# Optimization experiments

Hardware: AMD Instinct MI355X
Metric: run time of the kernel (lower is better)

Reference implementation:

```python
import jax, jax.numpy as jnp
import numpy as np

RES, RES_, STRIDE = 28, 14, 2
H, KD, AR = 8, 16, 4
SCALE = KD ** -0.5
EPS = 1e-5


def make_bias_idxs(res=RES, res_=RES_, stride=STRIDE):
    pts = [(i, j) for i in range(res) for j in range(res)]
    pts_ = [(i, j) for i in range(res_) for j in range(res_)]
    offs, idxs = {}, []
    for p1 in pts_:
        for p2 in pts:
            off = (abs(p1[0] * stride - p2[0]), abs(p1[1] * stride - p2[1]))
            if off not in offs:
                offs[off] = len(offs)
            idxs.append(offs[off])
    return np.array(idxs, dtype=np.int32).reshape(len(pts_), len(pts)), len(offs)


def setup_inputs() -> dict:
    key = jax.random.key(0)
    ks = jax.random.split(key, 16)
    idxs, n_off = make_bias_idxs()  # n_off == 784
    B, N, C = 128, RES * RES, 256
    d_kv, d_q, d_p, d_pin = 640, 128, 384, 512
    return {
        "hidden_state": jax.random.normal(ks[0], (B, N, C), jnp.float32),
        "w_kv": jax.random.normal(ks[1], (d_kv, C), jnp.float32) * 0.05,
        "kv_gamma": jax.random.uniform(ks[2], (d_kv,), jnp.float32, 0.5, 1.5),
        "kv_beta": jax.random.normal(ks[3], (d_kv,), jnp.float32) * 0.1,
        "kv_mean": jax.random.normal(ks[4], (d_kv,), jnp.float32) * 0.1,
        "kv_var": jax.random.uniform(ks[5], (d_kv,), jnp.float32, 0.5, 1.5),
        "w_q": jax.random.normal(ks[6], (d_q, C), jnp.float32) * 0.05,
        "q_gamma": jax.random.uniform(ks[7], (d_q,), jnp.float32, 0.5, 1.5),
        "q_beta": jax.random.normal(ks[8], (d_q,), jnp.float32) * 0.1,
        "q_mean": jax.random.normal(ks[9], (d_q,), jnp.float32) * 0.1,
        "q_var": jax.random.uniform(ks[10], (d_q,), jnp.float32, 0.5, 1.5),
        "w_proj": jax.random.normal(ks[11], (d_p, d_pin), jnp.float32) * 0.05,
        "p_gamma": jax.random.uniform(ks[12], (d_p,), jnp.float32, 0.5, 1.5),
        "p_beta": jax.random.normal(ks[13], (d_p,), jnp.float32) * 0.1,
        "p_mean": jax.random.normal(ks[14], (d_p,), jnp.float32) * 0.1,
        "p_var": jax.random.uniform(ks[15], (d_p,), jnp.float32, 0.5, 1.5),
        "attention_biases": jax.random.normal(jax.random.fold_in(key, 99), (H, n_off), jnp.float32),
        "attention_bias_idxs": jnp.asarray(idxs),
    }


def _bn(x, gamma, beta, mean, var):
    # eval-mode BatchNorm1d over last dim
    return (x - mean) * (gamma * jax.lax.rsqrt(var + EPS)) + beta


def _hardswish(x):
    return x * jnp.clip(x + 3.0, 0.0, 6.0) * (1.0 / 6.0)


def reference(hidden_state, w_kv, kv_gamma, kv_beta, kv_mean, kv_var,
              w_q, q_gamma, q_beta, q_mean, q_var,
              w_proj, p_gamma, p_beta, p_mean, p_var,
              attention_biases, attention_bias_idxs):
    B, N, C = hidden_state.shape
    N_ = RES_ * RES_
    # kv: [B, N, 640] -> key [B,H,N,KD], value [B,H,N,AR*KD]
    kv = _bn(hidden_state @ w_kv.T, kv_gamma, kv_beta, kv_mean, kv_var)
    kv = kv.reshape(B, N, H, KD + AR * KD)
    k = jnp.transpose(kv[..., :KD], (0, 2, 1, 3))          # [B,H,N,KD]
    v = jnp.transpose(kv[..., KD:], (0, 2, 1, 3))          # [B,H,N,AR*KD]
    # strided query subsample on the spatial grid
    hs = hidden_state.reshape(B, RES, RES, C)[:, ::STRIDE, ::STRIDE].reshape(B, N_, C)
    q = _bn(hs @ w_q.T, q_gamma, q_beta, q_mean, q_var)
    q = jnp.transpose(q.reshape(B, N_, H, KD), (0, 2, 1, 3))  # [B,H,N_,KD]
    bias = attention_biases[:, attention_bias_idxs]           # [H,N_,N] gathered
    attn = jnp.einsum('bhqd,bhkd->bhqk', q, k) * SCALE + bias
    attn = jax.nn.softmax(attn, axis=-1)
    out = jnp.einsum('bhqk,bhkd->bhqd', attn, v)              # [B,H,N_,AR*KD]
    out = jnp.transpose(out, (0, 2, 1, 3)).reshape(B, N_, H * AR * KD)
    out = _bn(_hardswish(out) @ w_proj.T, p_gamma, p_beta, p_mean, p_var)
    return out
```

## Files before the change

kernel.cpp:

```cpp
#include <hip/hip_runtime.h>

typedef _Float16 f16;
typedef __attribute__((ext_vector_type(2))) _Float16 f16x2;
typedef __attribute__((ext_vector_type(4))) _Float16 f16x4;
typedef __attribute__((ext_vector_type(8))) _Float16 f16x8;
typedef __attribute__((ext_vector_type(4))) float fvec4;
typedef __attribute__((ext_vector_type(4))) float f32x4;
typedef __attribute__((ext_vector_type(16))) float f32x16;
typedef __attribute__((ext_vector_type(4))) unsigned int uint4v;

#define NKEY 784
#define NKEYP 800
#define NQ 196
#define NQP 224
#define LOG2E 1.442695041f
#define SC2   0.360673760f
#define THR2  11.5415603f

static __device__ __forceinline__ f32x4 mfma16(f16x8 a, f16x8 b, f32x4 c) {
    return __builtin_amdgcn_mfma_f32_16x16x32_f16(a, b, c, 0, 0, 0);
}
static __device__ __forceinline__ f32x16 mfma32(f16x8 a, f16x8 b, f32x16 c) {
    return __builtin_amdgcn_mfma_f32_32x32x16_f16(a, b, c, 0, 0, 0);
}
static __device__ __forceinline__ unsigned pkrtz(float a, float b) {
    return __builtin_bit_cast(unsigned, __builtin_amdgcn_cvt_pkrtz(a, b));
}
static __device__ __forceinline__ f32x16 z16() {
    f32x16 v;
#pragma unroll
    for (int i = 0; i < 16; ++i) v[i] = 0.f;
    return v;
}

__global__ void prep_scales_all(const float* __restrict__ kg, const float* __restrict__ kb,
                                const float* __restrict__ km, const float* __restrict__ kvv,
                                const float* __restrict__ qg, const float* __restrict__ qb,
                                const float* __restrict__ qm, const float* __restrict__ qv,
                                const float* __restrict__ pg, const float* __restrict__ pb,
                                const float* __restrict__ pm, const float* __restrict__ pv,
                                float* __restrict__ sb) {
    int i = blockIdx.x * 256 + threadIdx.x;
    if (i < 640) {
        float s = kg[i] * rsqrtf(kvv[i] + 1e-5f);
        sb[i] = s; sb[640 + i] = kb[i] - km[i] * s;
    } else if (i < 768) {
        int j = i - 640;
        float s = qg[j] * rsqrtf(qv[j] + 1e-5f);
        sb[1280 + j] = s * SC2;
        sb[1408 + j] = (qb[j] - qm[j] * s) * SC2;
    } else if (i < 1152) {
        int j = i - 768;
        float s = pg[j] * rsqrtf(pv[j] + 1e-5f);
        sb[1536 + j] = s; sb[1920 + j] = pb[j] - pm[j] * s;
    }
}

__global__ void conv_w(const float* __restrict__ wkv, const float* __restrict__ wq,
                       const float* __restrict__ wp, f16* __restrict__ out) {
    int i = blockIdx.x * 256 + threadIdx.x;
    const float* src;
    f16* dst;
    int kc, n, K;
    if (i < 20480)      { int j = i;         kc = j / 640, n = j - kc * 640; src = wkv; dst = out + (size_t)j * 8;            K = 256; }
    else if (i < 24576) { int j = i - 20480; kc = j / 128, n = j - kc * 128; src = wq;  dst = out + 163840 + (size_t)j * 8;   K = 256; }
    else                { int j = i - 24576; kc = j / 384, n = j - kc * 384; src = wp;  dst = out + 196608 + (size_t)j * 8;   K = 512; }
    const float* s = src + (size_t)n * K + kc * 8;
    fvec4 v0 = *(const fvec4*)s;
    fvec4 v1 = *(const fvec4*)(s + 4);
    f16x8 h;
    h[0] = (f16)v0[0]; h[1] = (f16)v0[1]; h[2] = (f16)v0[2]; h[3] = (f16)v0[3];
    h[4] = (f16)v1[0]; h[5] = (f16)v1[1]; h[6] = (f16)v1[2]; h[7] = (f16)v1[3];
    *(f16x8*)dst = h;
}

__global__ void prep_bias(const float* __restrict__ biases, const int* __restrict__ idxs,
                          f16* __restrict__ biasS, int n_off) {
    int tid = blockIdx.x * 256 + threadIdx.x;
    const int r = tid & 15;
    const int lane = (tid >> 4) & 63;
    const int g = tid >> 10;
    const int kbk = g % 25;
    const int tmp = g / 25;
    const int qt = tmp % 7;
    const int h = tmp / 7;
    const int q = qt * 32 + (lane & 31);
    const int key = kbk * 32 + (r & 3) + 8 * (r >> 2) + 4 * (lane >> 5);
    float v;
    if (key >= NKEY)  v = -30000.f;
    else if (q < NQ)  v = biases[h * n_off + idxs[q * NKEY + key]] * LOG2E;
    else              v = 0.f;
    biasS[tid] = (f16)v;
}

template <int MODE>
__global__ __launch_bounds__(256) void gemm_db(
        const void* __restrict__ Ap, const f16x8* __restrict__ Wg,
        const float* __restrict__ sc, const float* __restrict__ sh,
        void* __restrict__ OutA, f16* __restrict__ OutV) {
    constexpr int K     = (MODE == 2) ? 512 : 256;
    constexpr int KS    = K / 32;
    constexpr int CHUNK = (MODE == 2) ? 16 : 32;
    constexpr int NFR   = CHUNK / 16;
    constexpr int NT    = (MODE == 0) ? 640 : (MODE == 1 ? 128 : 384);
    constexpr int NCH   = (MODE == 0) ? 20 : (MODE == 1 ? 4 : 12);
    constexpr int UNITS = (K / 8) * CHUNK;
    constexpr int SR    = UNITS / 256;

    __shared__ f16x8 Wl[2][UNITS];

    const int t = threadIdx.x;
    const int lane = t & 63, wid = t >> 6;
    const int fr = lane & 15, kg = lane >> 4;
    const int m0 = blockIdx.x * 64;
    const int nb0 = blockIdx.y * (NCH * CHUNK);
    const int mrow = m0 + wid * 16 + fr;

    size_t arow;
    if constexpr (MODE == 1) {
        int b = mrow / 196, nn = mrow - b * 196;
        arow = (size_t)b * 784 + (nn / 14) * 56 + (nn % 14) * 2;
    } else {
        arow = (size_t)mrow;
    }
    f16x8 af[KS];
#pragma unroll
    for (int ks = 0; ks < KS; ++ks) {
        if constexpr (MODE == 2) {
            af[ks] = *(const f16x8*)((const f16*)Ap + arow * K + ks * 32 + kg * 8);
        } else {
            const float* a = (const float*)Ap + arow * 256 + ks * 32 + kg * 8;
            fvec4 v0 = *(const fvec4*)a;
            fvec4 v1 = *(const fvec4*)(a + 4);
            f16x8 hv;
            hv[0] = (f16)v0[0]; hv[1] = (f16)v0[1]; hv[2] = (f16)v0[2]; hv[3] = (f16)v0[3];
            hv[4] = (f16)v1[0]; hv[5] = (f16)v1[1]; hv[6] = (f16)v1[2]; hv[7] = (f16)v1[3];
            af[ks] = hv;
        }
    }

#pragma unroll
    for (int rr = 0; rr < SR; ++rr) {
        const int idx = rr * 256 + t;
        Wl[0][idx] = Wg[(size_t)(idx / CHUNK) * NT + nb0 + (idx % CHUNK)];
    }
    __syncthreads();

    const int rg = kg * 4;
    int cur = 0;
    for (int c = 0; c < NCH; ++c) {
        const int n0c = nb0 + c * CHUNK;

        f16x8 nx0, nx1, nx2, nx3;
        if (c + 1 < NCH) {
            const int n0n = n0c + CHUNK;
            nx0 = Wg[(size_t)((0 * 256 + t) / CHUNK) * NT + n0n + ((0 * 256 + t) % CHUNK)];
            if constexpr (SR > 1)
                nx1 = Wg[(size_t)((1 * 256 + t) / CHUNK) * NT + n0n + ((1 * 256 + t) % CHUNK)];
            if constexpr (SR > 2) {
                nx2 = Wg[(size_t)((2 * 256 + t) / CHUNK) * NT + n0n + ((2 * 256 + t) % CHUNK)];
                nx3 = Wg[(size_t)((3 * 256 + t) / CHUNK) * NT + n0n + ((3 * 256 + t) % CHUNK)];
            }
        }

        f32x4 acc[NFR];
#pragma unroll
        for (int j = 0; j < NFR; ++j) acc[j] = (f32x4){0.f, 0.f, 0.f, 0.f};
#pragma unroll
        for (int ks = 0; ks < KS; ++ks) {
            f16x8 bfr[NFR];
#pragma unroll
            for (int nf = 0; nf < NFR; ++nf)
                bfr[nf] = Wl[cur][(ks * 4 + kg) * CHUNK + nf * 16 + fr];
#pragma unroll
            for (int nf = 0; nf < NFR; ++nf)
                acc[nf] = mfma16(af[ks], bfr[nf], acc[nf]);
        }

        const int mbase = m0 + wid * 16 + rg;
#pragma unroll
        for (int nf = 0; nf < NFR; ++nf) {
            const int n = n0c + nf * 16 + fr;
            const float scn = sc[n], shn = sh[n];
            if constexpr (MODE == 0) {
                const int b = mbase / 784;
                const int nn = mbase - b * 784;
                const int hd = n / 80;
                const int cc = n - hd * 80;
                const size_t bh = (size_t)(b * 8 + hd);
                if (cc < 16) {
#pragma unroll
                    for (int r = 0; r < 4; ++r) {
                        float y = acc[nf][r] * scn + shn;
                        ((f16*)OutA)[(bh * NKEYP + nn + r) * 16 + cc] = (f16)y;
                    }
                } else {
                    const int kbk = nn >> 5, sH = (nn >> 4) & 1;
                    const int kq = (nn >> 2) & 3;
                    const int slot = ((((kq & 1) << 1) | (kq >> 1)) << 2) | (nn & 3);
                    f16x4 pv;
#pragma unroll
                    for (int r = 0; r < 4; ++r) pv[r] = (f16)(acc[nf][r] * scn + shn);
                    *(f16x4*)(OutV + ((bh * 25 + kbk) * 2 + sH) * 1024 + (cc - 16) * 16 + slot) = pv;
                }
            } else if constexpr (MODE == 1) {
                const int b = mbase / 196;
                const int nn = mbase - b * 196;
                const int hd = n >> 4, cc = n & 15;
                const size_t bh = (size_t)(b * 8 + hd);
#pragma unroll
                for (int r = 0; r < 4; ++r) {
                    float y = acc[nf][r] * scn + shn;
                    ((f16*)OutA)[(bh * NQP + nn + r) * 16 + cc] = (f16)y;
                }
            } else {
#pragma unroll
                for (int r = 0; r < 4; ++r) {
                    float y = acc[nf][r] * scn + shn;
                    ((float*)OutA)[(size_t)(mbase + r) * 384 + n] = y;
                }
            }
        }

        if (c + 1 < NCH) {
            Wl[cur ^ 1][0 * 256 + t] = nx0;
            if constexpr (SR > 1)
                Wl[cur ^ 1][1 * 256 + t] = nx1;
            if constexpr (SR > 2) {
                Wl[cur ^ 1][2 * 256 + t] = nx2;
                Wl[cur ^ 1][3 * 256 + t] = nx3;
            }
            __syncthreads();
            cur ^= 1;
        }
    }
}

__global__ __launch_bounds__(448) void attn_fused(const f16* __restrict__ kb,
                                                  const f16* __restrict__ vtb,
                                                  const f16* __restrict__ qw,
                                                  const f16* __restrict__ biasS,
                                                  f16* __restrict__ ao) {
    const int bh = blockIdx.x;
    const int b = bh >> 3, h = bh & 7;
    const int wid = threadIdx.x >> 6;
    const int lane = threadIdx.x & 63;
    const int l31 = lane & 31;
    const int hh = lane >> 5;
    const int q0 = wid * 32;

    const f16x8 bq = *(const f16x8*)(qw + ((size_t)bh * NQP + q0 + l31) * 16 + hh * 8);
    const f16* kpp = kb + (size_t)bh * (NKEYP * 16) + (size_t)l31 * 16 + hh * 8;
    const f16* cbp = biasS + ((size_t)(h * 7 + wid) * 25 * 64 + lane) * 16;
    const f16* vkb = vtb + (size_t)bh * 51200 + l31 * 16 + hh * 8;

    float mrun = -1e30f;
    float lsum = 0.f;
    f32x16 o0 = z16(), o1 = z16();

    f32x16 sn;
    {
        const f16x8* bp = (const f16x8*)cbp;
        f16x8 b0 = bp[0], b1 = bp[1];
        f32x16 ci;
#pragma unroll
        for (int r = 0; r < 8; ++r) { ci[r] = (float)b0[r]; ci[8 + r] = (float)b1[r]; }
        sn = mfma32(*(const f16x8*)kpp, bq, ci);
    }

#pragma unroll 1
    for (int kbi = 0; kbi < 25; ++kbi) {
        f32x16 s = sn;
        if (kbi + 1 < 25) {
            kpp += 512; cbp += 1024;
            const f16x8* bp = (const f16x8*)cbp;
            f16x8 b0 = bp[0], b1 = bp[1];
            f32x16 ci;
#pragma unroll
            for (int r = 0; r < 8; ++r) { ci[r] = (float)b0[r]; ci[8 + r] = (float)b1[r]; }
            sn = mfma32(*(const f16x8*)kpp, bq, ci);
        }
        f16x8 bv00 = *(const f16x8*)(vkb);
        f16x8 bv01 = *(const f16x8*)(vkb + 512);
        f16x8 bv10 = *(const f16x8*)(vkb + 1024);
        f16x8 bv11 = *(const f16x8*)(vkb + 1536);
        vkb += 2048;

        float m0v = fmaxf(fmaxf(s[0], s[1]), fmaxf(s[2], s[3]));
        float m1v = fmaxf(fmaxf(s[4], s[5]), fmaxf(s[6], s[7]));
        float m2v = fmaxf(fmaxf(s[8], s[9]), fmaxf(s[10], s[11]));
        float m3v = fmaxf(fmaxf(s[12], s[13]), fmaxf(s[14], s[15]));
        float cmax = fmaxf(fmaxf(m0v, m1v), fmaxf(m2v, m3v));
        cmax = fmaxf(cmax, __shfl_xor(cmax, 32));
        if (__any(cmax > mrun + THR2)) {
            float mnew = fmaxf(mrun, cmax);
            float f = exp2f(mrun - mnew);
            mrun = mnew;
            lsum *= f;
#pragma unroll
            for (int r = 0; r < 16; ++r) {
                const int cr = (r & 3) + ((r >> 2) << 3) + (hh << 2);
                float fr2 = __shfl(f, cr);
                o0[r] *= fr2;
                o1[r] *= fr2;
            }
        }
        float pr[16];
        float psum = 0.f;
#pragma unroll
        for (int r = 0; r < 16; ++r) {
            pr[r] = exp2f(s[r] - mrun);
            psum += pr[r];
        }
        lsum += psum;
        uint4v w0, w1;
        w0[0] = pkrtz(pr[0], pr[1]);   w0[1] = pkrtz(pr[2], pr[3]);
        w0[2] = pkrtz(pr[4], pr[5]);   w0[3] = pkrtz(pr[6], pr[7]);
        w1[0] = pkrtz(pr[8], pr[9]);   w1[1] = pkrtz(pr[10], pr[11]);
        w1[2] = pkrtz(pr[12], pr[13]); w1[3] = pkrtz(pr[14], pr[15]);
        f16x8 pa0 = __builtin_bit_cast(f16x8, w0);
        f16x8 pa1 = __builtin_bit_cast(f16x8, w1);
        o0 = mfma32(pa0, bv00, o0);
        o1 = mfma32(pa0, bv01, o1);
        o0 = mfma32(pa1, bv10, o0);
        o1 = mfma32(pa1, bv11, o1);
    }
    lsum += __shfl_xor(lsum, 32);
    const float inv = 1.0f / lsum;
#pragma unroll
    for (int r = 0; r < 16; ++r) {
        const int cr = (r & 3) + ((r >> 2) << 3) + (hh << 2);
        const float iq = __shfl(inv, cr);
        const int qg = q0 + cr;
        if (qg < NQ) {
            float v0 = o0[r] * iq, v1 = o1[r] * iq;
            float h0 = v0 * fminf(fmaxf(v0 + 3.f, 0.f), 6.f) * (1.f / 6.f);
            float h1 = v1 * fminf(fmaxf(v1 + 3.f, 0.f), 6.f) * (1.f / 6.f);
            f16* dst = ao + ((size_t)b * NQ + qg) * 512 + h * 64 + l31;
            dst[0] = (f16)h0;
            dst[32] = (f16)h1;
        }
    }
}

extern "C" void kernel_launch(void* const* d_in, const int* in_sizes, int n_in,
                              void* d_out, int out_size, void* d_ws, size_t ws_size,
                              hipStream_t stream) {
    (void)n_in; (void)out_size; (void)ws_size;
    const float* hidden = (const float*)d_in[0];
    const float* w_kv   = (const float*)d_in[1];
    const float* w_q    = (const float*)d_in[6];
    const float* w_p    = (const float*)d_in[11];
    const float* biases = (const float*)d_in[16];
    const int*   idxs   = (const int*)d_in[17];
    const int n_off = in_sizes[16] / 8;

    char* ws = (char*)d_ws;
    const size_t OFF_K  = 0;
    const size_t OFF_V  = 26214400;
    const size_t OFF_Q  = 131072000;
    const size_t OFF_AO = 138412032;
    const size_t OFF_W  = 164102144;
    const size_t OFF_SC = 164888576;
    const size_t OFF_BT = 164897792;
    f16*   kbuf  = (f16*)(ws + OFF_K);
    f16*   vbuf  = (f16*)(ws + OFF_V);
    f16*   qbuf  = (f16*)(ws + OFF_Q);
    f16*   aobuf = (f16*)(ws + OFF_AO);
    f16*   wf16  = (f16*)(ws + OFF_W);
    float* scbuf = (float*)(ws + OFF_SC);
    f16*   btbuf = (f16*)(ws + OFF_BT);

    prep_scales_all<<<5, 256, 0, stream>>>(
        (const float*)d_in[2], (const float*)d_in[3], (const float*)d_in[4], (const float*)d_in[5],
        (const float*)d_in[7], (const float*)d_in[8], (const float*)d_in[9], (const float*)d_in[10],
        (const float*)d_in[12], (const float*)d_in[13], (const float*)d_in[14], (const float*)d_in[15],
        scbuf);
    conv_w<<<192, 256, 0, stream>>>(w_kv, w_q, w_p, wf16);
    prep_bias<<<5600, 256, 0, stream>>>(biases, idxs, btbuf, n_off);
    hipMemsetAsync(qbuf, 0, (size_t)1024 * NQP * 16 * 2, stream);
    gemm_db<0><<<dim3(1568, 1), 256, 0, stream>>>(hidden, (const f16x8*)wf16, scbuf, scbuf + 640, kbuf, vbuf);
    gemm_db<1><<<dim3(392, 1), 256, 0, stream>>>(hidden, (const f16x8*)(wf16 + 163840), scbuf + 1280, scbuf + 1408, qbuf, nullptr);
    attn_fused<<<1024, 448, 0, stream>>>(kbuf, vbuf, qbuf, btbuf, aobuf);
    gemm_db<2><<<dim3(392, 2), 256, 0, stream>>>(aobuf, (const f16x8*)(wf16 + 196608), scbuf + 1536, scbuf + 1920, d_out, nullptr);
}
```

Baseline: 210.6 us.

## Fuse KV projection GEMM into attention kernel per batch and head pair

```diff
diff --git a/kernel.cpp b/kernel.cpp
--- a/kernel.cpp
+++ b/kernel.cpp
@@ -97,13 +97,13 @@
 __global__ __launch_bounds__(256) void gemm_db(
         const void* __restrict__ Ap, const f16x8* __restrict__ Wg,
         const float* __restrict__ sc, const float* __restrict__ sh,
-        void* __restrict__ OutA, f16* __restrict__ OutV) {
+        void* __restrict__ OutA) {
     constexpr int K     = (MODE == 2) ? 512 : 256;
     constexpr int KS    = K / 32;
     constexpr int CHUNK = (MODE == 2) ? 16 : 32;
     constexpr int NFR   = CHUNK / 16;
-    constexpr int NT    = (MODE == 0) ? 640 : (MODE == 1 ? 128 : 384);
-    constexpr int NCH   = (MODE == 0) ? 20 : (MODE == 1 ? 4 : 12);
+    constexpr int NT    = (MODE == 1) ? 128 : 384;
+    constexpr int NCH   = (MODE == 1) ? 4 : 12;
     constexpr int UNITS = (K / 8) * CHUNK;
     constexpr int SR    = UNITS / 256;
 
@@ -182,28 +182,7 @@
         for (int nf = 0; nf < NFR; ++nf) {
             const int n = n0c + nf * 16 + fr;
             const float scn = sc[n], shn = sh[n];
-            if constexpr (MODE == 0) {
-                const int b = mbase / 784;
-                const int nn = mbase - b * 784;
-                const int hd = n / 80;
-                const int cc = n - hd * 80;
-                const size_t bh = (size_t)(b * 8 + hd);
-                if (cc < 16) {
-#pragma unroll
-                    for (int r = 0; r < 4; ++r) {
-                        float y = acc[nf][r] * scn + shn;
-                        ((f16*)OutA)[(bh * NKEYP + nn + r) * 16 + cc] = (f16)y;
-                    }
-                } else {
-                    const int kbk = nn >> 5, sH = (nn >> 4) & 1;
-                    const int kq = (nn >> 2) & 3;
-                    const int slot = ((((kq & 1) << 1) | (kq >> 1)) << 2) | (nn & 3);
-                    f16x4 pv;
-#pragma unroll
-                    for (int r = 0; r < 4; ++r) pv[r] = (f16)(acc[nf][r] * scn + shn);
-                    *(f16x4*)(OutV + ((bh * 25 + kbk) * 2 + sH) * 1024 + (cc - 16) * 16 + slot) = pv;
-                }
-            } else if constexpr (MODE == 1) {
+            if constexpr (MODE == 1) {
                 const int b = mbase / 196;
                 const int nn = mbase - b * 196;
                 const int hd = n >> 4, cc = n & 15;
@@ -236,43 +215,118 @@
     }
 }
 
-__global__ __launch_bounds__(448) void attn_fused(const f16* __restrict__ kb,
-                                                  const f16* __restrict__ vtb,
-                                                  const f16* __restrict__ qw,
-                                                  const f16* __restrict__ biasS,
-                                                  f16* __restrict__ ao) {
-    const int bh = blockIdx.x;
-    const int b = bh >> 3, h = bh & 7;
-    const int wid = threadIdx.x >> 6;
-    const int lane = threadIdx.x & 63;
+__global__ __launch_bounds__(448) void kv_attn(
+        const float* __restrict__ hidden, const f16x8* __restrict__ Wg,
+        const float* __restrict__ sc, const float* __restrict__ sh,
+        const f16* __restrict__ qw, const f16* __restrict__ biasS,
+        f16* __restrict__ kbuf, f16* __restrict__ vbuf, f16* __restrict__ ao) {
+    const int x = blockIdx.x & 7, y = blockIdx.x >> 3;
+    const int hp = y & 3;
+    const int b = (y >> 2) * 8 + x;
+    const int t = threadIdx.x;
+    const int lane = t & 63, wid = t >> 6;
+    const int fr = lane & 15, kg = lane >> 4;
+    const int rg = kg * 4;
+    const int nb0 = hp * 160;
+
+    __shared__ f16x8 Wl[2][1024];
+
+    for (int p = 0; p < 7; ++p) {
+        const int mrow = p * 112 + wid * 16 + fr;
+        const float* abase = hidden + ((size_t)b * 784 + mrow) * 256 + kg * 8;
+        f16x8 af[8];
+#pragma unroll
+        for (int ks = 0; ks < 8; ++ks) {
+            fvec4 v0 = *(const fvec4*)(abase + ks * 32);
+            fvec4 v1 = *(const fvec4*)(abase + ks * 32 + 4);
+            f16x8 hv;
+            hv[0] = (f16)v0[0]; hv[1] = (f16)v0[1]; hv[2] = (f16)v0[2]; hv[3] = (f16)v0[3];
+            hv[4] = (f16)v1[0]; hv[5] = (f16)v1[1]; hv[6] = (f16)v1[2]; hv[7] = (f16)v1[3];
+            af[ks] = hv;
+        }
+        __syncthreads();
+        Wl[0][t]       = Wg[(size_t)(t / 32) * 640 + nb0 + (t % 32)];
+        Wl[0][t + 448] = Wg[(size_t)((t + 448) / 32) * 640 + nb0 + ((t + 448) % 32)];
+        if (t < 128)
+            Wl[0][t + 896] = Wg[(size_t)((t + 896) / 32) * 640 + nb0 + ((t + 896) % 32)];
+        __syncthreads();
+
+        int cur = 0;
+        for (int c = 0; c < 5; ++c) {
+            const int n0c = nb0 + c * 32;
+            f16x8 nx0, nx1, nx2;
+            if (c + 1 < 5) {
+                const int n0n = n0c + 32;
+                nx0 = Wg[(size_t)(t / 32) * 640 + n0n + (t % 32)];
+                nx1 = Wg[(size_t)((t + 448) / 32) * 640 + n0n + ((t + 448) % 32)];
+                if (t < 128)
+                    nx2 = Wg[(size_t)((t + 896) / 32) * 640 + n0n + ((t + 896) % 32)];
+            }
+            f32x4 acc0 = (f32x4){0.f, 0.f, 0.f, 0.f};
+            f32x4 acc1 = (f32x4){0.f, 0.f, 0.f, 0.f};
+#pragma unroll
+            for (int ks = 0; ks < 8; ++ks) {
+                f16x8 b0 = Wl[cur][(ks * 4 + kg) * 32 + fr];
+                f16x8 b1 = Wl[cur][(ks * 4 + kg) * 32 + 16 + fr];
+                acc0 = mfma16(af[ks], b0, acc0);
+                acc1 = mfma16(af[ks], b1, acc1);
+            }
+            const int mbase = p * 112 + wid * 16 + rg;
+#pragma unroll
+            for (int nf = 0; nf < 2; ++nf) {
+                const f32x4 a4 = nf ? acc1 : acc0;
+                const int n = n0c + nf * 16 + fr;
+                const float scn = sc[n], shn = sh[n];
+                const int hd = n / 80;
+                const int cc = n - hd * 80;
+                const size_t bh = (size_t)(b * 8 + hd);
+                if (cc < 16) {
+#pragma unroll
+                    for (int r = 0; r < 4; ++r) {
+                        float yv = a4[r] * scn + shn;
+                        kbuf[(bh * NKEYP + mbase + r) * 16 + cc] = (f16)yv;
+                    }
+                } else {
+                    const int kbk = mbase >> 5, sH = (mbase >> 4) & 1;
+                    const int kq = (mbase >> 2) & 3;
+                    const int slot = ((((kq & 1) << 1) | (kq >> 1)) << 2) | (mbase & 3);
+                    f16x4 pv;
+#pragma unroll
+                    for (int r = 0; r < 4; ++r) pv[r] = (f16)(a4[r] * scn + shn);
+                    *(f16x4*)(vbuf + ((bh * 25 + kbk) * 2 + sH) * 1024 + (cc - 16) * 16 + slot) = pv;
+                }
+            }
+            if (c + 1 < 5) {
+                Wl[cur ^ 1][t] = nx0;
+                Wl[cur ^ 1][t + 448] = nx1;
+                if (t < 128) Wl[cur ^ 1][t + 896] = nx2;
+                __syncthreads();
+                cur ^= 1;
+            }
+        }
+    }
+    __syncthreads();
+
     const int l31 = lane & 31;
     const int hh = lane >> 5;
-    const int q0 = wid * 32;
-
-    const f16x8 bq = *(const f16x8*)(qw + ((size_t)bh * NQP + q0 + l31) * 16 + hh * 8);
-    const f16* kpp = kb + (size_t)bh * (NKEYP * 16) + (size_t)l31 * 16 + hh * 8;
-    const f16* cbp = biasS + ((size_t)(h * 7 + wid) * 25 * 64 + lane) * 16;
-    const f16* vkb = vtb + (size_t)bh * 51200 + l31 * 16 + hh * 8;
-
-    float mrun = -1e30f;
-    float lsum = 0.f;
-    f32x16 o0 = z16(), o1 = z16();
-
-    f32x16 sn;
-    {
-        const f16x8* bp = (const f16x8*)cbp;
-        f16x8 b0 = bp[0], b1 = bp[1];
-        f32x16 ci;
-#pragma unroll
-        for (int r = 0; r < 8; ++r) { ci[r] = (float)b0[r]; ci[8 + r] = (float)b1[r]; }
-        sn = mfma32(*(const f16x8*)kpp, bq, ci);
-    }
+    const int qt = wid;
+    const int q0 = qt * 32;
 
 #pragma unroll 1
-    for (int kbi = 0; kbi < 25; ++kbi) {
-        f32x16 s = sn;
-        if (kbi + 1 < 25) {
-            kpp += 512; cbp += 1024;
+    for (int u = 0; u < 2; ++u) {
+        const int h = hp * 2 + u;
+        const int bh = b * 8 + h;
+        const f16x8 bq = *(const f16x8*)(qw + ((size_t)bh * NQP + q0 + l31) * 16 + hh * 8);
+        const f16* kpp = kbuf + (size_t)bh * (NKEYP * 16) + (size_t)l31 * 16 + hh * 8;
+        const f16* cbp = biasS + ((size_t)(h * 7 + qt) * 25 * 64 + lane) * 16;
+        const f16* vkb = vbuf + (size_t)bh * 51200 + l31 * 16 + hh * 8;
+
+        float mrun = -1e30f;
+        float lsum = 0.f;
+        f32x16 o0 = z16(), o1 = z16();
+
+        f32x16 sn;
+        {
             const f16x8* bp = (const f16x8*)cbp;
             f16x8 b0 = bp[0], b1 = bp[1];
             f32x16 ci;
@@ -280,65 +334,79 @@
             for (int r = 0; r < 8; ++r) { ci[r] = (float)b0[r]; ci[8 + r] = (float)b1[r]; }
             sn = mfma32(*(const f16x8*)kpp, bq, ci);
         }
-        f16x8 bv00 = *(const f16x8*)(vkb);
-        f16x8 bv01 = *(const f16x8*)(vkb + 512);
-        f16x8 bv10 = *(const f16x8*)(vkb + 1024);
-        f16x8 bv11 = *(const f16x8*)(vkb + 1536);
-        vkb += 2048;
-
-        float m0v = fmaxf(fmaxf(s[0], s[1]), fmaxf(s[2], s[3]));
-        float m1v = fmaxf(fmaxf(s[4], s[5]), fmaxf(s[6], s[7]));
-        float m2v = fmaxf(fmaxf(s[8], s[9]), fmaxf(s[10], s[11]));
-        float m3v = fmaxf(fmaxf(s[12], s[13]), fmaxf(s[14], s[15]));
-        float cmax = fmaxf(fmaxf(m0v, m1v), fmaxf(m2v, m3v));
-        cmax = fmaxf(cmax, __shfl_xor(cmax, 32));
-        if (__any(cmax > mrun + THR2)) {
-            float mnew = fmaxf(mrun, cmax);
-            float f = exp2f(mrun - mnew);
-            mrun = mnew;
-            lsum *= f;
+
+#pragma unroll 1
+        for (int kbi = 0; kbi < 25; ++kbi) {
+            f32x16 s = sn;
+            if (kbi + 1 < 25) {
+                kpp += 512; cbp += 1024;
+                const f16x8* bp = (const f16x8*)cbp;
+                f16x8 b0 = bp[0], b1 = bp[1];
+                f32x16 ci;
+#pragma unroll
+                for (int r = 0; r < 8; ++r) { ci[r] = (float)b0[r]; ci[8 + r] = (float)b1[r]; }
+                sn = mfma32(*(const f16x8*)kpp, bq, ci);
+            }
+            f16x8 bv00 = *(const f16x8*)(vkb);
+            f16x8 bv01 = *(const f16x8*)(vkb + 512);
+            f16x8 bv10 = *(const f16x8*)(vkb + 1024);
+            f16x8 bv11 = *(const f16x8*)(vkb + 1536);
+            vkb += 2048;
+
+            float m0v = fmaxf(fmaxf(s[0], s[1]), fmaxf(s[2], s[3]));
+            float m1v = fmaxf(fmaxf(s[4], s[5]), fmaxf(s[6], s[7]));
+            float m2v = fmaxf(fmaxf(s[8], s[9]), fmaxf(s[10], s[11]));
+            float m3v = fmaxf(fmaxf(s[12], s[13]), fmaxf(s[14], s[15]));
+            float cmax = fmaxf(fmaxf(m0v, m1v), fmaxf(m2v, m3v));
+            cmax = fmaxf(cmax, __shfl_xor(cmax, 32));
+            if (__any(cmax > mrun + THR2)) {
+                float mnew = fmaxf(mrun, cmax);
+                float f = exp2f(mrun - mnew);
+                mrun = mnew;
+                lsum *= f;
+#pragma unroll
+                for (int r = 0; r < 16; ++r) {
+                    const int cr = (r & 3) + ((r >> 2) << 3) + (hh << 2);
+                    float fr2 = __shfl(f, cr);
+                    o0[r] *= fr2;
+                    o1[r] *= fr2;
+                }
+            }
+            float pr[16];
+            float psum = 0.f;
 #pragma unroll
             for (int r = 0; r < 16; ++r) {
-                const int cr = (r & 3) + ((r >> 2) << 3) + (hh << 2);
-                float fr2 = __shfl(f, cr);
-                o0[r] *= fr2;
-                o1[r] *= fr2;
-            }
-        }
-        float pr[16];
-        float psum = 0.f;
+                pr[r] = exp2f(s[r] - mrun);
+                psum += pr[r];
+            }
+            lsum += psum;
+            uint4v w0, w1;
+            w0[0] = pkrtz(pr[0], pr[1]);   w0[1] = pkrtz(pr[2], pr[3]);
+            w0[2] = pkrtz(pr[4], pr[5]);   w0[3] = pkrtz(pr[6], pr[7]);
+            w1[0] = pkrtz(pr[8], pr[9]);   w1[1] = pkrtz(pr[10], pr[11]);
+            w1[2] = pkrtz(pr[12], pr[13]); w1[3] = pkrtz(pr[14], pr[15]);
+            f16x8 pa0 = __builtin_bit_cast(f16x8, w0);
+            f16x8 pa1 = __builtin_bit_cast(f16x8, w1);
+            o0 = mfma32(pa0, bv00, o0);
+            o1 = mfma32(pa0, bv01, o1);
+            o0 = mfma32(pa1, bv10, o0);
+            o1 = mfma32(pa1, bv11, o1);
+        }
+        lsum += __shfl_xor(lsum, 32);
+        const float inv = 1.0f / lsum;
 #pragma unroll
         for (int r = 0; r < 16; ++r) {
-            pr[r] = exp2f(s[r] - mrun);
-            psum += pr[r];
-        }
-        lsum += psum;
-        uint4v w0, w1;
-        w0[0] = pkrtz(pr[0], pr[1]);   w0[1] = pkrtz(pr[2], pr[3]);
-        w0[2] = pkrtz(pr[4], pr[5]);   w0[3] = pkrtz(pr[6], pr[7]);
-        w1[0] = pkrtz(pr[8], pr[9]);   w1[1] = pkrtz(pr[10], pr[11]);
-        w1[2] = pkrtz(pr[12], pr[13]); w1[3] = pkrtz(pr[14], pr[15]);
-        f16x8 pa0 = __builtin_bit_cast(f16x8, w0);
-        f16x8 pa1 = __builtin_bit_cast(f16x8, w1);
-        o0 = mfma32(pa0, bv00, o0);
-        o1 = mfma32(pa0, bv01, o1);
-        o0 = mfma32(pa1, bv10, o0);
-        o1 = mfma32(pa1, bv11, o1);
-    }
-    lsum += __shfl_xor(lsum, 32);
-    const float inv = 1.0f / lsum;
-#pragma unroll
-    for (int r = 0; r < 16; ++r) {
-        const int cr = (r & 3) + ((r >> 2) << 3) + (hh << 2);
-        const float iq = __shfl(inv, cr);
-        const int qg = q0 + cr;
-        if (qg < NQ) {
-            float v0 = o0[r] * iq, v1 = o1[r] * iq;
-            float h0 = v0 * fminf(fmaxf(v0 + 3.f, 0.f), 6.f) * (1.f / 6.f);
-            float h1 = v1 * fminf(fmaxf(v1 + 3.f, 0.f), 6.f) * (1.f / 6.f);
-            f16* dst = ao + ((size_t)b * NQ + qg) * 512 + h * 64 + l31;
-            dst[0] = (f16)h0;
-            dst[32] = (f16)h1;
+            const int cr = (r & 3) + ((r >> 2) << 3) + (hh << 2);
+            const float iq = __shfl(inv, cr);
+            const int qg = q0 + cr;
+            if (qg < NQ) {
+                float v0 = o0[r] * iq, v1 = o1[r] * iq;
+                float h0 = v0 * fminf(fmaxf(v0 + 3.f, 0.f), 6.f) * (1.f / 6.f);
+                float h1 = v1 * fminf(fmaxf(v1 + 3.f, 0.f), 6.f) * (1.f / 6.f);
+                f16* dst = ao + ((size_t)b * NQ + qg) * 512 + h * 64 + l31;
+                dst[0] = (f16)h0;
+                dst[32] = (f16)h1;
+            }
         }
     }
 }
@@ -379,8 +447,8 @@
     conv_w<<<192, 256, 0, stream>>>(w_kv, w_q, w_p, wf16);
     prep_bias<<<5600, 256, 0, stream>>>(biases, idxs, btbuf, n_off);
     hipMemsetAsync(qbuf, 0, (size_t)1024 * NQP * 16 * 2, stream);
-    gemm_db<0><<<dim3(1568, 1), 256, 0, stream>>>(hidden, (const f16x8*)wf16, scbuf, scbuf + 640, kbuf, vbuf);
-    gemm_db<1><<<dim3(392, 1), 256, 0, stream>>>(hidden, (const f16x8*)(wf16 + 163840), scbuf + 1280, scbuf + 1408, qbuf, nullptr);
-    attn_fused<<<1024, 448, 0, stream>>>(kbuf, vbuf, qbuf, btbuf, aobuf);
-    gemm_db<2><<<dim3(392, 2), 256, 0, stream>>>(aobuf, (const f16x8*)(wf16 + 196608), scbuf + 1536, scbuf + 1920, d_out, nullptr);
-}
+    gemm_db<1><<<dim3(392, 1), 256, 0, stream>>>(hidden, (const f16x8*)(wf16 + 163840), scbuf + 1280, scbuf + 1408, qbuf);
+    kv_attn<<<512, 448, 0, stream>>>(hidden, (const f16x8*)wf16, scbuf, scbuf + 640,
+                                     qbuf, btbuf, kbuf, vbuf, aobuf);
+    gemm_db<2><<<dim3(392, 2), 256, 0, stream>>>(aobuf, (const f16x8*)(wf16 + 196608), scbuf + 1536, scbuf + 1920, d_out);
+}
```

Measured after the change: 252.9 us. +20.1%, slower.
